# Kernel tuning notes

Hardware: AMD Instinct MI355X
Metric: run time of the kernel (lower is better)

Reference implementation:

```python
import jax, jax.numpy as jnp
import numpy as np

N = 100000
E = 1600000
F_IN = 128
DIM = 32
NUM_CLASSES = 40
BN_EPS = 1e-5


def setup_inputs() -> dict:
    key = jax.random.key(0)
    ks = jax.random.split(key, 16)
    inp = {}
    inp['x'] = jax.random.normal(ks[0], (N, F_IN), dtype=jnp.float32)
    inp['edge_index'] = jax.random.randint(ks[1], (2, E), 0, N, dtype=jnp.int64)
    s = lambda fan_in: 1.0 / np.sqrt(fan_in)
    # GINConv 1 MLP: Linear(F_IN, DIM) -> ReLU -> Linear(DIM, DIM)
    inp['w1a'] = jax.random.uniform(ks[2], (F_IN, DIM), jnp.float32, -s(F_IN), s(F_IN))
    inp['b1a'] = jnp.zeros((DIM,), jnp.float32)
    inp['w1b'] = jax.random.uniform(ks[3], (DIM, DIM), jnp.float32, -s(DIM), s(DIM))
    inp['b1b'] = jnp.zeros((DIM,), jnp.float32)
    # GINConv 2 MLP: Linear(DIM, DIM) -> ReLU -> Linear(DIM, DIM)
    inp['w2a'] = jax.random.uniform(ks[4], (DIM, DIM), jnp.float32, -s(DIM), s(DIM))
    inp['b2a'] = jnp.zeros((DIM,), jnp.float32)
    inp['w2b'] = jax.random.uniform(ks[5], (DIM, DIM), jnp.float32, -s(DIM), s(DIM))
    inp['b2b'] = jnp.zeros((DIM,), jnp.float32)
    # BatchNorm params (eval mode: running stats)
    inp['bn1_g'] = jnp.ones((DIM,), jnp.float32)
    inp['bn1_b'] = jnp.zeros((DIM,), jnp.float32)
    inp['bn1_m'] = jax.random.normal(ks[6], (DIM,), jnp.float32) * 0.1
    inp['bn1_v'] = jax.random.uniform(ks[7], (DIM,), jnp.float32, 0.5, 1.5)
    inp['bn2_g'] = jnp.ones((DIM,), jnp.float32)
    inp['bn2_b'] = jnp.zeros((DIM,), jnp.float32)
    inp['bn2_m'] = jax.random.normal(ks[8], (DIM,), jnp.float32) * 0.1
    inp['bn2_v'] = jax.random.uniform(ks[9], (DIM,), jnp.float32, 0.5, 1.5)
    # FC heads
    inp['fc1_w'] = jax.random.uniform(ks[10], (DIM, DIM), jnp.float32, -s(DIM), s(DIM))
    inp['fc1_b'] = jnp.zeros((DIM,), jnp.float32)
    inp['fc2_w'] = jax.random.uniform(ks[11], (DIM, NUM_CLASSES), jnp.float32, -s(DIM), s(DIM))
    inp['fc2_b'] = jnp.zeros((NUM_CLASSES,), jnp.float32)
    return inp


def _gin_conv(x, src, dst, wa, ba, wb, bb):
    # sum-aggregate neighbor features (messages flow src -> dst), eps = 0
    agg = jax.ops.segment_sum(x[src], dst, num_segments=N)
    h = agg + x  # (1 + eps) * x + sum_j x_j
    h = jax.nn.relu(h @ wa + ba)
    return h @ wb + bb


def _bn(x, g, b, m, v):
    return (x - m) * (g * jax.lax.rsqrt(v + BN_EPS)) + b


def reference(x, edge_index, w1a, b1a, w1b, b1b, w2a, b2a, w2b, b2b,
              bn1_g, bn1_b, bn1_m, bn1_v, bn2_g, bn2_b, bn2_m, bn2_v,
              fc1_w, fc1_b, fc2_w, fc2_b):
    src, dst = edge_index[0], edge_index[1]
    h = jax.nn.relu(_gin_conv(x, src, dst, w1a, b1a, w1b, b1b))
    h = _bn(h, bn1_g, bn1_b, bn1_m, bn1_v)  # dropout is identity in eval
    h = _gin_conv(h, src, dst, w2a, b2a, w2b, b2b)
    h = _bn(h, bn2_g, bn2_b, bn2_m, bn2_v)
    h = jax.nn.relu(h @ fc1_w + fc1_b)
    logits = h @ fc2_w + fc2_b
    return jax.nn.log_softmax(logits, axis=1)
```

## Files before the change

kernel.cpp:

```cpp
#include <hip/hip_runtime.h>
#include <hip/hip_bf16.h>

static constexpr int N_   = 100000;
static constexpr int E_   = 1600000;
static constexpr int FIN_ = 128;
static constexpr int DIM_ = 32;
static constexpr int NC_  = 40;
static constexpr int NB_BKT = (N_ + 127) / 128;
static constexpr int NCHUNK = 256;
static constexpr int EPC    = E_ / NCHUNK;
static constexpr int PROJ_NB = N_ / 32;
static constexpr int CS_NB  = (NB_BKT + 7) / 8;

__device__ __forceinline__ int edge_at(const void* e, int is64, long long i) {
    return is64 ? (int)((const long long*)e)[i] : ((const int*)e)[i];
}

__device__ __forceinline__ float bflo(unsigned u) { return __uint_as_float(u << 16); }
__device__ __forceinline__ float bfhi(unsigned u) { return __uint_as_float(u & 0xffff0000u); }

#define DETECT_FLAG(edge, sflag)                                        \
    if (threadIdx.x < 64) {                                             \
        const long long* p_ = (const long long*)(edge);                 \
        long long v_ = p_[threadIdx.x];                                 \
        bool bad_ = (v_ < 0 || v_ >= (long long)N_);                    \
        unsigned long long m_ = __ballot(bad_);                         \
        if (threadIdx.x == 0) sflag = (m_ == 0ull) ? 1 : 0;             \
    }                                                                   \
    __syncthreads();

__global__ __launch_bounds__(256) void chist_kernel(const void* __restrict__ edge,
                                                    int* __restrict__ ghist) {
    __shared__ int lh[NB_BKT];
    __shared__ int sflag;
    DETECT_FLAG(edge, sflag)
    for (int i = threadIdx.x; i < NB_BKT; i += 256) lh[i] = 0;
    __syncthreads();
    int f = sflag;
    int b = blockIdx.x;
    int end = b * EPC + EPC;
    for (int e = b * EPC + threadIdx.x; e < end; e += 256) {
        int d = edge_at(edge, f, (long long)E_ + e);
        atomicAdd(&lh[d >> 7], 1);
    }
    __syncthreads();
    for (int i = threadIdx.x; i < NB_BKT; i += 256) ghist[b * NB_BKT + i] = lh[i];
}

__global__ __launch_bounds__(256) void colscan_kernel(const int* __restrict__ ghist,
                                                      int* __restrict__ gcur,
                                                      int* __restrict__ bcnt,
                                                      int* __restrict__ bbase,
                                                      int* __restrict__ offs,
                                                      int* __restrict__ done) {
    __shared__ int tile[256 * 9];
    __shared__ int a[256];
    __shared__ int lastFlag;
    int tid = threadIdx.x;
    int k0 = blockIdx.x * 8;

    {
        int kk = tid & 7, r0 = tid >> 3;
        for (int p = 0; p < 8; ++p) {
            int b = r0 + p * 32;
            int k = k0 + kk;
            tile[b * 9 + kk] = (k < NB_BKT) ? ghist[b * NB_BKT + k] : 0;
        }
    }
    __syncthreads();

    int c = tid >> 5, lane = tid & 31;
    int v[8]; int s = 0;
#pragma unroll
    for (int r = 0; r < 8; ++r) { v[r] = tile[(lane * 8 + r) * 9 + c]; s += v[r]; }
    int incl = s;
#pragma unroll
    for (int off = 1; off < 32; off <<= 1) {
        int u = __shfl_up(incl, off, 32);
        if (lane >= off) incl += u;
    }
    int ex = incl - s;
    int k = k0 + c;
    if (k < NB_BKT) {
        int run = ex;
#pragma unroll
        for (int r = 0; r < 8; ++r) {
            int b = lane * 8 + r;
            gcur[b * NB_BKT + k] = run;
            run += v[r];
        }
        if (lane == 31) bcnt[k] = run;
    }
    __syncthreads();
    if (tid == 0) {
        __threadfence();
        int old = atomicAdd(done, 1);
        lastFlag = (old == CS_NB - 1) ? 1 : 0;
    }
    __syncthreads();
    if (lastFlag) {
        __threadfence();
        int b4[4]; int base4 = tid * 4; int t = 0;
#pragma unroll
        for (int j = 0; j < 4; ++j) { int i = base4 + j; b4[j] = (i < NB_BKT) ? bcnt[i] : 0; t += b4[j]; }
        a[tid] = t;
        __syncthreads();
        for (int off = 1; off < 256; off <<= 1) {
            int u = a[tid] + ((tid >= off) ? a[tid - off] : 0);
            __syncthreads(); a[tid] = u; __syncthreads();
        }
        int g = a[tid] - t;
#pragma unroll
        for (int j = 0; j < 4; ++j) { int i = base4 + j; if (i < NB_BKT) bbase[i] = g; g += b4[j]; }
        if (tid == 255) offs[N_] = a[255];
    }
}

__global__ __launch_bounds__(256) void dscatter_kernel(const void* __restrict__ edge,
                                                       const int* __restrict__ bbase,
                                                       const int* __restrict__ gcur,
                                                       int* __restrict__ packed) {
    __shared__ int cur[NB_BKT];
    __shared__ int sflag;
    DETECT_FLAG(edge, sflag)
    int b = blockIdx.x, tid = threadIdx.x;
    for (int k = tid; k < NB_BKT; k += 256) cur[k] = bbase[k] + gcur[b * NB_BKT + k];
    __syncthreads();
    int f = sflag;
    int end = b * EPC + EPC;
    for (int e = b * EPC + tid; e < end; e += 256) {
        int s = edge_at(edge, f, e);
        int d = edge_at(edge, f, (long long)E_ + e);
        int pos = atomicAdd(&cur[d >> 7], 1);
        packed[pos] = s | ((d & 127) << 17);
    }
}

__global__ __launch_bounds__(256) void fat_kernel(const int* __restrict__ bcnt,
                                                  const int* __restrict__ bbase,
                                                  const int* __restrict__ packed,
                                                  int* __restrict__ offs,
                                                  int* __restrict__ csr,
                                                  const float* __restrict__ x,
                                                  const float* __restrict__ w,
                                                  __hip_bfloat16* __restrict__ yh) {
    __shared__ __align__(16) char smem[32768];
    int tid = threadIdx.x;
    if (blockIdx.x < NB_BKT) {
        int* c   = (int*)smem;
        int* cur = (int*)smem + 128;
        int b = blockIdx.x;
        int beg = bbase[b], cnt = bcnt[b];
        if (tid < 128) c[tid] = 0;
        __syncthreads();
        for (int i = tid; i < cnt; i += 256)
            atomicAdd(&c[packed[beg + i] >> 17], 1);
        __syncthreads();
        int myv = (tid < 128) ? c[tid] : 0;
        for (int off = 1; off < 128; off <<= 1) {
            int t = 0;
            if (tid < 128) t = c[tid] + ((tid >= off) ? c[tid - off] : 0);
            __syncthreads();
            if (tid < 128) c[tid] = t;
            __syncthreads();
        }
        if (tid < 128) {
            int ex = c[tid] - myv;
            cur[tid] = ex;
            int node = b * 128 + tid;
            if (node < N_) offs[node] = beg + ex;
        }
        __syncthreads();
        for (int i = tid; i < cnt; i += 256) {
            int v = packed[beg + i];
            int p = atomicAdd(&cur[v >> 17], 1);
            csr[beg + p] = v & 0x1FFFF;
        }
    } else {
        float* wsm = (float*)smem;
        float* xs  = (float*)(smem + 16384);
        const float4* w4 = (const float4*)w;
        float4* ws4 = (float4*)wsm;
        for (int i = tid; i < FIN_ * DIM_ / 4; i += 256) ws4[i] = w4[i];

        int nodeBase = (blockIdx.x - NB_BKT) * 32;
        const float4* x4 = (const float4*)(x + (size_t)nodeBase * FIN_);
        float4* xs4 = (float4*)xs;
        for (int i = tid; i < 32 * FIN_ / 4; i += 256) xs4[i] = x4[i];
        __syncthreads();

        int d = tid & 31, ns = tid >> 5;
        float acc0 = 0.f, acc1 = 0.f, acc2 = 0.f, acc3 = 0.f;
        const float4* r0 = (const float4*)&xs[(ns +  0) * FIN_];
        const float4* r1 = (const float4*)&xs[(ns +  8) * FIN_];
        const float4* r2 = (const float4*)&xs[(ns + 16) * FIN_];
        const float4* r3 = (const float4*)&xs[(ns + 24) * FIN_];
#pragma unroll
        for (int kc = 0; kc < FIN_ / 4; ++kc) {
            float w0 = wsm[(kc * 4 + 0) * DIM_ + d];
            float w1 = wsm[(kc * 4 + 1) * DIM_ + d];
            float w2 = wsm[(kc * 4 + 2) * DIM_ + d];
            float w3 = wsm[(kc * 4 + 3) * DIM_ + d];
            float4 a;
            a = r0[kc]; acc0 += a.x * w0 + a.y * w1 + a.z * w2 + a.w * w3;
            a = r1[kc]; acc1 += a.x * w0 + a.y * w1 + a.z * w2 + a.w * w3;
            a = r2[kc]; acc2 += a.x * w0 + a.y * w1 + a.z * w2 + a.w * w3;
            a = r3[kc]; acc3 += a.x * w0 + a.y * w1 + a.z * w2 + a.w * w3;
        }
        __hip_bfloat16* yo = yh + (size_t)nodeBase * DIM_ + d;
        yo[(ns +  0) * DIM_] = __float2bfloat16(acc0);
        yo[(ns +  8) * DIM_] = __float2bfloat16(acc1);
        yo[(ns + 16) * DIM_] = __float2bfloat16(acc2);
        yo[(ns + 24) * DIM_] = __float2bfloat16(acc3);
    }
}

__device__ __forceinline__ void gather_row(const int* __restrict__ csr,
                                           const char* __restrict__ vb,
                                           int beg, int end, int loff,
                                           float& a0, float& a1, float& a2, float& a3) {
    int i = beg;
    for (; i + 3 < end; i += 4) {
        int s0 = csr[i], s1 = csr[i + 1], s2 = csr[i + 2], s3 = csr[i + 3];
        uint2 u0 = *(const uint2*)(vb + (((size_t)s0) << 6) + loff);
        uint2 u1 = *(const uint2*)(vb + (((size_t)s1) << 6) + loff);
        uint2 u2 = *(const uint2*)(vb + (((size_t)s2) << 6) + loff);
        uint2 u3 = *(const uint2*)(vb + (((size_t)s3) << 6) + loff);
        a0 += (bflo(u0.x) + bflo(u1.x)) + (bflo(u2.x) + bflo(u3.x));
        a1 += (bfhi(u0.x) + bfhi(u1.x)) + (bfhi(u2.x) + bfhi(u3.x));
        a2 += (bflo(u0.y) + bflo(u1.y)) + (bflo(u2.y) + bflo(u3.y));
        a3 += (bfhi(u0.y) + bfhi(u1.y)) + (bfhi(u2.y) + bfhi(u3.y));
    }
    for (; i < end; ++i) {
        int s0 = csr[i];
        uint2 u0 = *(const uint2*)(vb + (((size_t)s0) << 6) + loff);
        a0 += bflo(u0.x); a1 += bfhi(u0.x); a2 += bflo(u0.y); a3 += bfhi(u0.y);
    }
}

__global__ __launch_bounds__(256) void aggmlp1_kernel(const int* __restrict__ offs,
                                                      const int* __restrict__ csr,
                                                      const __hip_bfloat16* __restrict__ yh,
                                                      const float* __restrict__ b1a,
                                                      const float* __restrict__ w1b,
                                                      const float* __restrict__ b1b,
                                                      const float* __restrict__ g1,
                                                      const float* __restrict__ be1,
                                                      const float* __restrict__ m1,
                                                      const float* __restrict__ v1,
                                                      const float* __restrict__ w2a,
                                                      __hip_bfloat16* __restrict__ zh) {
    __shared__ __align__(16) float A[32 * 36];
    __shared__ __align__(16) float B[32 * 36];
    __shared__ float w1s[DIM_ * DIM_];
    __shared__ float w2s[DIM_ * DIM_];
    int tid = threadIdx.x;
    for (int i = tid; i < DIM_ * DIM_; i += 256) { w1s[i] = w1b[i]; w2s[i] = w2a[i]; }

    int nl = tid >> 3, lane = tid & 7;
    int node = blockIdx.x * 32 + nl;
    int beg = offs[node], end = offs[node + 1];
    float a0 = 0.f, a1 = 0.f, a2 = 0.f, a3 = 0.f;
    gather_row(csr, (const char*)yh, beg, end, lane << 3, a0, a1, a2, a3);
    {
        float* p = &A[nl * 36 + lane * 4];
        p[0] = a0; p[1] = a1; p[2] = a2; p[3] = a3;
    }
    __syncthreads();

    int d = tid & 31, ng = tid >> 5;
    size_t gbase = (size_t)blockIdx.x * 32 * DIM_;

    {
        float bv = b1a[d];
#pragma unroll
        for (int r = 0; r < 4; ++r) {
            int n = r * 8 + ng;
            float yv = __bfloat162float(yh[gbase + n * DIM_ + d]);
            A[n * 36 + d] = fmaxf(A[n * 36 + d] + yv + bv, 0.f);
        }
    }
    __syncthreads();

    float sc1 = g1[d] * rsqrtf(v1[d] + 1e-5f);
    float sh1 = be1[d] - m1[d] * sc1;

    {
        float s0 = b1b[d], s1 = s0, s2 = s0, s3 = s0;
        const float4* r0 = (const float4*)&A[(ng +  0) * 36];
        const float4* r1 = (const float4*)&A[(ng +  8) * 36];
        const float4* r2 = (const float4*)&A[(ng + 16) * 36];
        const float4* r3 = (const float4*)&A[(ng + 24) * 36];
#pragma unroll
        for (int kc = 0; kc < 8; ++kc) {
            float w0 = w1s[(kc * 4 + 0) * DIM_ + d];
            float w1 = w1s[(kc * 4 + 1) * DIM_ + d];
            float w2 = w1s[(kc * 4 + 2) * DIM_ + d];
            float w3 = w1s[(kc * 4 + 3) * DIM_ + d];
            float4 a;
            a = r0[kc]; s0 += a.x * w0 + a.y * w1 + a.z * w2 + a.w * w3;
            a = r1[kc]; s1 += a.x * w0 + a.y * w1 + a.z * w2 + a.w * w3;
            a = r2[kc]; s2 += a.x * w0 + a.y * w1 + a.z * w2 + a.w * w3;
            a = r3[kc]; s3 += a.x * w0 + a.y * w1 + a.z * w2 + a.w * w3;
        }
        B[(ng +  0) * 36 + d] = fmaxf(s0, 0.f) * sc1 + sh1;
        B[(ng +  8) * 36 + d] = fmaxf(s1, 0.f) * sc1 + sh1;
        B[(ng + 16) * 36 + d] = fmaxf(s2, 0.f) * sc1 + sh1;
        B[(ng + 24) * 36 + d] = fmaxf(s3, 0.f) * sc1 + sh1;
    }
    __syncthreads();

    {
        float s0 = 0.f, s1 = 0.f, s2 = 0.f, s3 = 0.f;
        const float4* r0 = (const float4*)&B[(ng +  0) * 36];
        const float4* r1 = (const float4*)&B[(ng +  8) * 36];
        const float4* r2 = (const float4*)&B[(ng + 16) * 36];
        const float4* r3 = (const float4*)&B[(ng + 24) * 36];
#pragma unroll
        for (int kc = 0; kc < 8; ++kc) {
            float w0 = w2s[(kc * 4 + 0) * DIM_ + d];
            float w1 = w2s[(kc * 4 + 1) * DIM_ + d];
            float w2 = w2s[(kc * 4 + 2) * DIM_ + d];
            float w3 = w2s[(kc * 4 + 3) * DIM_ + d];
            float4 a;
            a = r0[kc]; s0 += a.x * w0 + a.y * w1 + a.z * w2 + a.w * w3;
            a = r1[kc]; s1 += a.x * w0 + a.y * w1 + a.z * w2 + a.w * w3;
            a = r2[kc]; s2 += a.x * w0 + a.y * w1 + a.z * w2 + a.w * w3;
            a = r3[kc]; s3 += a.x * w0 + a.y * w1 + a.z * w2 + a.w * w3;
        }
        zh[gbase + (ng +  0) * DIM_ + d] = __float2bfloat16(s0);
        zh[gbase + (ng +  8) * DIM_ + d] = __float2bfloat16(s1);
        zh[gbase + (ng + 16) * DIM_ + d] = __float2bfloat16(s2);
        zh[gbase + (ng + 24) * DIM_ + d] = __float2bfloat16(s3);
    }
}

__global__ __launch_bounds__(256) void aggmlp2_kernel(const int* __restrict__ offs,
                                                      const int* __restrict__ csr,
                                                      const __hip_bfloat16* __restrict__ zh,
                                                      const float* __restrict__ b2a,
                                                      const float* __restrict__ w2b,
                                                      const float* __restrict__ b2b,
                                                      const float* __restrict__ g2,
                                                      const float* __restrict__ be2,
                                                      const float* __restrict__ m2,
                                                      const float* __restrict__ v2,
                                                      const float* __restrict__ f1w,
                                                      const float* __restrict__ f1b,
                                                      const float* __restrict__ f2w,
                                                      const float* __restrict__ f2b,
                                                      float* __restrict__ out) {
    __shared__ __align__(16) float A[32 * 36];
    __shared__ __align__(16) float BC[DIM_ * NC_];
    __shared__ float wA[DIM_ * DIM_];
    __shared__ float wB[DIM_ * DIM_];
    int tid = threadIdx.x;
    for (int i = tid; i < DIM_ * DIM_; i += 256) { wA[i] = w2b[i]; wB[i] = f1w[i]; }

    int nl = tid >> 3, lane = tid & 7;
    int node = blockIdx.x * 32 + nl;
    int beg = offs[node], end = offs[node + 1];
    float a0 = 0.f, a1 = 0.f, a2 = 0.f, a3 = 0.f;
    gather_row(csr, (const char*)zh, beg, end, lane << 3, a0, a1, a2, a3);
    {
        float* p = &A[nl * 36 + lane * 4];
        p[0] = a0; p[1] = a1; p[2] = a2; p[3] = a3;
    }
    __syncthreads();

    int d = tid & 31, ng = tid >> 5;
    size_t gbase = (size_t)blockIdx.x * 32 * DIM_;

    {
        float bv = b2a[d];
#pragma unroll
        for (int r = 0; r < 4; ++r) {
            int n = r * 8 + ng;
            float zv = __bfloat162float(zh[gbase + n * DIM_ + d]);
            A[n * 36 + d] = fmaxf(A[n * 36 + d] + zv + bv, 0.f);
        }
    }
    __syncthreads();

    float sc2 = g2[d] * rsqrtf(v2[d] + 1e-5f);
    float sh2 = be2[d] - m2[d] * sc2;

    {
        float s0 = b2b[d], s1 = s0, s2 = s0, s3 = s0;
        const float4* r0 = (const float4*)&A[(ng +  0) * 36];
        const float4* r1 = (const float4*)&A[(ng +  8) * 36];
        const float4* r2 = (const float4*)&A[(ng + 16) * 36];
        const float4* r3 = (const float4*)&A[(ng + 24) * 36];
#pragma unroll
        for (int kc = 0; kc < 8; ++kc) {
            float w0 = wA[(kc * 4 + 0) * DIM_ + d];
            float w1 = wA[(kc * 4 + 1) * DIM_ + d];
            float w2 = wA[(kc * 4 + 2) * DIM_ + d];
            float w3 = wA[(kc * 4 + 3) * DIM_ + d];
            float4 a;
            a = r0[kc]; s0 += a.x * w0 + a.y * w1 + a.z * w2 + a.w * w3;
            a = r1[kc]; s1 += a.x * w0 + a.y * w1 + a.z * w2 + a.w * w3;
            a = r2[kc]; s2 += a.x * w0 + a.y * w1 + a.z * w2 + a.w * w3;
            a = r3[kc]; s3 += a.x * w0 + a.y * w1 + a.z * w2 + a.w * w3;
        }
        BC[(ng +  0) * 36 + d] = s0 * sc2 + sh2;
        BC[(ng +  8) * 36 + d] = s1 * sc2 + sh2;
        BC[(ng + 16) * 36 + d] = s2 * sc2 + sh2;
        BC[(ng + 24) * 36 + d] = s3 * sc2 + sh2;
    }
    __syncthreads();

    {
        float s0 = f1b[d], s1 = s0, s2 = s0, s3 = s0;
        const float4* r0 = (const float4*)&BC[(ng +  0) * 36];
        const float4* r1 = (const float4*)&BC[(ng +  8) * 36];
        const float4* r2 = (const float4*)&BC[(ng + 16) * 36];
        const float4* r3 = (const float4*)&BC[(ng + 24) * 36];
#pragma unroll
        for (int kc = 0; kc < 8; ++kc) {
            float w0 = wB[(kc * 4 + 0) * DIM_ + d];
            float w1 = wB[(kc * 4 + 1) * DIM_ + d];
            float w2 = wB[(kc * 4 + 2) * DIM_ + d];
            float w3 = wB[(kc * 4 + 3) * DIM_ + d];
            float4 a;
            a = r0[kc]; s0 += a.x * w0 + a.y * w1 + a.z * w2 + a.w * w3;
            a = r1[kc]; s1 += a.x * w0 + a.y * w1 + a.z * w2 + a.w * w3;
            a = r2[kc]; s2 += a.x * w0 + a.y * w1 + a.z * w2 + a.w * w3;
            a = r3[kc]; s3 += a.x * w0 + a.y * w1 + a.z * w2 + a.w * w3;
        }
        A[(ng +  0) * 36 + d] = fmaxf(s0, 0.f);
        A[(ng +  8) * 36 + d] = fmaxf(s1, 0.f);
        A[(ng + 16) * 36 + d] = fmaxf(s2, 0.f);
        A[(ng + 24) * 36 + d] = fmaxf(s3, 0.f);
    }
    __syncthreads();
    for (int i = tid; i < DIM_ * NC_; i += 256) BC[i] = f2w[i];
    __syncthreads();

    int c2 = 32 + (d & 7);
    float l00 = f2b[d], l01 = l00, l02 = l00, l03 = l00;
    float cb = f2b[c2];
    float l10 = cb, l11 = cb, l12 = cb, l13 = cb;
    {
        const float4* r0 = (const float4*)&A[(ng +  0) * 36];
        const float4* r1 = (const float4*)&A[(ng +  8) * 36];
        const float4* r2 = (const float4*)&A[(ng + 16) * 36];
        const float4* r3 = (const float4*)&A[(ng + 24) * 36];
#pragma unroll
        for (int kc = 0; kc < 8; ++kc) {
            float wa0 = BC[(kc * 4 + 0) * NC_ + d];
            float wa1 = BC[(kc * 4 + 1) * NC_ + d];
            float wa2 = BC[(kc * 4 + 2) * NC_ + d];
            float wa3 = BC[(kc * 4 + 3) * NC_ + d];
            float wb0 = BC[(kc * 4 + 0) * NC_ + c2];
            float wb1 = BC[(kc * 4 + 1) * NC_ + c2];
            float wb2 = BC[(kc * 4 + 2) * NC_ + c2];
            float wb3 = BC[(kc * 4 + 3) * NC_ + c2];
            float4 a;
            a = r0[kc];
            l00 += a.x * wa0 + a.y * wa1 + a.z * wa2 + a.w * wa3;
            l10 += a.x * wb0 + a.y * wb1 + a.z * wb2 + a.w * wb3;
            a = r1[kc];
            l01 += a.x * wa0 + a.y * wa1 + a.z * wa2 + a.w * wa3;
            l11 += a.x * wb0 + a.y * wb1 + a.z * wb2 + a.w * wb3;
            a = r2[kc];
            l02 += a.x * wa0 + a.y * wa1 + a.z * wa2 + a.w * wa3;
            l12 += a.x * wb0 + a.y * wb1 + a.z * wb2 + a.w * wb3;
            a = r3[kc];
            l03 += a.x * wa0 + a.y * wa1 + a.z * wa2 + a.w * wa3;
            l13 += a.x * wb0 + a.y * wb1 + a.z * wb2 + a.w * wb3;
        }
    }
#pragma unroll
    for (int r = 0; r < 4; ++r) {
        float l0 = (r == 0) ? l00 : (r == 1) ? l01 : (r == 2) ? l02 : l03;
        float l1 = (r == 0) ? l10 : (r == 1) ? l11 : (r == 2) ? l12 : l13;
        int n = r * 8 + ng;
        float mx = fmaxf(l0, l1);
#pragma unroll
        for (int off = 16; off; off >>= 1) mx = fmaxf(mx, __shfl_xor(mx, off));
        float se = __expf(l0 - mx) + ((d < 8) ? __expf(l1 - mx) : 0.f);
#pragma unroll
        for (int off = 16; off; off >>= 1) se += __shfl_xor(se, off);
        float lse = mx + __logf(se);
        size_t ob = (size_t)(blockIdx.x * 32 + n) * NC_;
        out[ob + d] = l0 - lse;
        if (d < 8) out[ob + 32 + d] = l1 - lse;
    }
}

extern "C" void kernel_launch(void* const* d_in, const int* in_sizes, int n_in,
                              void* d_out, int out_size, void* d_ws, size_t ws_size,
                              hipStream_t stream) {
    const float* x   = (const float*)d_in[0];
    const void*  edg = d_in[1];
    const float* w1a = (const float*)d_in[2];
    const float* b1a = (const float*)d_in[3];
    const float* w1b = (const float*)d_in[4];
    const float* b1b = (const float*)d_in[5];
    const float* w2a = (const float*)d_in[6];
    const float* b2a = (const float*)d_in[7];
    const float* w2b = (const float*)d_in[8];
    const float* b2b = (const float*)d_in[9];
    const float* g1  = (const float*)d_in[10];
    const float* be1 = (const float*)d_in[11];
    const float* m1  = (const float*)d_in[12];
    const float* v1  = (const float*)d_in[13];
    const float* g2  = (const float*)d_in[14];
    const float* be2 = (const float*)d_in[15];
    const float* m2  = (const float*)d_in[16];
    const float* v2  = (const float*)d_in[17];
    const float* f1w = (const float*)d_in[18];
    const float* f1b = (const float*)d_in[19];
    const float* f2w = (const float*)d_in[20];
    const float* f2b = (const float*)d_in[21];
    float* out = (float*)d_out;

    char* ws = (char*)d_ws;
    int* done   = (int*)ws;
    int* bcnt   = (int*)(ws + 256);
    int* bbase  = (int*)(ws + 3584);
    int* ghist  = (int*)(ws + 6912);
    int* gcur   = (int*)(ws + 807680);
    int* offs   = (int*)(ws + 1608448);
    int* packed = (int*)(ws + 2008576);
    int* csr    = (int*)(ws + 8408576);
    __hip_bfloat16* yh = (__hip_bfloat16*)(ws + 14808576);
    __hip_bfloat16* zh = (__hip_bfloat16*)(ws + 21208576);

    hipMemsetAsync(done, 0, 4, stream);

    chist_kernel<<<NCHUNK, 256, 0, stream>>>(edg, ghist);
    colscan_kernel<<<CS_NB, 256, 0, stream>>>(ghist, gcur, bcnt, bbase, offs, done);
    dscatter_kernel<<<NCHUNK, 256, 0, stream>>>(edg, bbase, gcur, packed);
    fat_kernel<<<NB_BKT + PROJ_NB, 256, 0, stream>>>(bcnt, bbase, packed, offs, csr,
                                                     x, w1a, yh);

    aggmlp1_kernel<<<N_ / 32, 256, 0, stream>>>(offs, csr, yh, b1a, w1b, b1b,
                                                g1, be1, m1, v1, w2a, zh);

    aggmlp2_kernel<<<N_ / 32, 256, 0, stream>>>(offs, csr, zh, b2a, w2b, b2b,
                                                g2, be2, m2, v2, f1w, f1b,
                                                f2w, f2b, out);
}
```

Before: 312.6 us.

## Split fused gather+MLP kernels into separate gather and MLP kernels

Each fused aggregate+MLP kernel is split in two. A lightweight gather kernel sums neighbour rows, adds the self row and bias, applies ReLU and writes fp32 rows to a workspace buffer. A separate MLP kernel then reads those rows into shared memory. The gather kernel uses no shared memory or weight loads, which may raise occupancy for the latency-bound gather, at the cost of two extra launches and an extra 12.8 MB fp32 write and read per layer.

```diff
diff --git a/kernel.cpp b/kernel.cpp
--- a/kernel.cpp
+++ b/kernel.cpp
@@ -238,49 +238,50 @@
     }
 }
 
-__global__ __launch_bounds__(256) void aggmlp1_kernel(const int* __restrict__ offs,
-                                                      const int* __restrict__ csr,
-                                                      const __hip_bfloat16* __restrict__ yh,
-                                                      const float* __restrict__ b1a,
-                                                      const float* __restrict__ w1b,
-                                                      const float* __restrict__ b1b,
-                                                      const float* __restrict__ g1,
-                                                      const float* __restrict__ be1,
-                                                      const float* __restrict__ m1,
-                                                      const float* __restrict__ v1,
-                                                      const float* __restrict__ w2a,
-                                                      __hip_bfloat16* __restrict__ zh) {
+__global__ __launch_bounds__(256) void gathu_kernel(const int* __restrict__ offs,
+                                                    const int* __restrict__ csr,
+                                                    const __hip_bfloat16* __restrict__ vh,
+                                                    const float* __restrict__ bias,
+                                                    float* __restrict__ u) {
+    int tid = threadIdx.x;
+    int nl = tid >> 3, slot = tid & 7;
+    int node = blockIdx.x * 32 + nl;
+    int beg = offs[node], end = offs[node + 1];
+    float a0 = 0.f, a1 = 0.f, a2 = 0.f, a3 = 0.f;
+    gather_row(csr, (const char*)vh, beg, end, slot << 3, a0, a1, a2, a3);
+    uint2 uy = *(const uint2*)((const char*)vh + (((size_t)node) << 6) + (slot << 3));
+    float4 bv = ((const float4*)bias)[slot];
+    float4 r;
+    r.x = fmaxf(a0 + bflo(uy.x) + bv.x, 0.f);
+    r.y = fmaxf(a1 + bfhi(uy.x) + bv.y, 0.f);
+    r.z = fmaxf(a2 + bflo(uy.y) + bv.z, 0.f);
+    r.w = fmaxf(a3 + bfhi(uy.y) + bv.w, 0.f);
+    ((float4*)u)[(size_t)blockIdx.x * 256 + tid] = r;
+}
+
+__global__ __launch_bounds__(256) void mlp1_kernel(const float* __restrict__ u,
+                                                   const float* __restrict__ w1b,
+                                                   const float* __restrict__ b1b,
+                                                   const float* __restrict__ g1,
+                                                   const float* __restrict__ be1,
+                                                   const float* __restrict__ m1,
+                                                   const float* __restrict__ v1,
+                                                   const float* __restrict__ w2a,
+                                                   __hip_bfloat16* __restrict__ zh) {
     __shared__ __align__(16) float A[32 * 36];
     __shared__ __align__(16) float B[32 * 36];
     __shared__ float w1s[DIM_ * DIM_];
     __shared__ float w2s[DIM_ * DIM_];
     int tid = threadIdx.x;
     for (int i = tid; i < DIM_ * DIM_; i += 256) { w1s[i] = w1b[i]; w2s[i] = w2a[i]; }
-
-    int nl = tid >> 3, lane = tid & 7;
-    int node = blockIdx.x * 32 + nl;
-    int beg = offs[node], end = offs[node + 1];
-    float a0 = 0.f, a1 = 0.f, a2 = 0.f, a3 = 0.f;
-    gather_row(csr, (const char*)yh, beg, end, lane << 3, a0, a1, a2, a3);
-    {
-        float* p = &A[nl * 36 + lane * 4];
-        p[0] = a0; p[1] = a1; p[2] = a2; p[3] = a3;
+    {
+        int n = tid >> 3, sl = tid & 7;
+        *(float4*)&A[n * 36 + sl * 4] = ((const float4*)u)[(size_t)blockIdx.x * 256 + tid];
     }
     __syncthreads();
 
     int d = tid & 31, ng = tid >> 5;
     size_t gbase = (size_t)blockIdx.x * 32 * DIM_;
-
-    {
-        float bv = b1a[d];
-#pragma unroll
-        for (int r = 0; r < 4; ++r) {
-            int n = r * 8 + ng;
-            float yv = __bfloat162float(yh[gbase + n * DIM_ + d]);
-            A[n * 36 + d] = fmaxf(A[n * 36 + d] + yv + bv, 0.f);
-        }
-    }
-    __syncthreads();
 
     float sc1 = g1[d] * rsqrtf(v1[d] + 1e-5f);
     float sh1 = be1[d] - m1[d] * sc1;
@@ -335,52 +336,31 @@
     }
 }
 
-__global__ __launch_bounds__(256) void aggmlp2_kernel(const int* __restrict__ offs,
-                                                      const int* __restrict__ csr,
-                                                      const __hip_bfloat16* __restrict__ zh,
-                                                      const float* __restrict__ b2a,
-                                                      const float* __restrict__ w2b,
-                                                      const float* __restrict__ b2b,
-                                                      const float* __restrict__ g2,
-                                                      const float* __restrict__ be2,
-                                                      const float* __restrict__ m2,
-                                                      const float* __restrict__ v2,
-                                                      const float* __restrict__ f1w,
-                                                      const float* __restrict__ f1b,
-                                                      const float* __restrict__ f2w,
-                                                      const float* __restrict__ f2b,
-                                                      float* __restrict__ out) {
+__global__ __launch_bounds__(256) void mlp2_kernel(const float* __restrict__ u,
+                                                   const float* __restrict__ w2b,
+                                                   const float* __restrict__ b2b,
+                                                   const float* __restrict__ g2,
+                                                   const float* __restrict__ be2,
+                                                   const float* __restrict__ m2,
+                                                   const float* __restrict__ v2,
+                                                   const float* __restrict__ f1w,
+                                                   const float* __restrict__ f1b,
+                                                   const float* __restrict__ f2w,
+                                                   const float* __restrict__ f2b,
+                                                   float* __restrict__ out) {
     __shared__ __align__(16) float A[32 * 36];
     __shared__ __align__(16) float BC[DIM_ * NC_];
     __shared__ float wA[DIM_ * DIM_];
     __shared__ float wB[DIM_ * DIM_];
     int tid = threadIdx.x;
     for (int i = tid; i < DIM_ * DIM_; i += 256) { wA[i] = w2b[i]; wB[i] = f1w[i]; }
-
-    int nl = tid >> 3, lane = tid & 7;
-    int node = blockIdx.x * 32 + nl;
-    int beg = offs[node], end = offs[node + 1];
-    float a0 = 0.f, a1 = 0.f, a2 = 0.f, a3 = 0.f;
-    gather_row(csr, (const char*)zh, beg, end, lane << 3, a0, a1, a2, a3);
-    {
-        float* p = &A[nl * 36 + lane * 4];
-        p[0] = a0; p[1] = a1; p[2] = a2; p[3] = a3;
+    {
+        int n = tid >> 3, sl = tid & 7;
+        *(float4*)&A[n * 36 + sl * 4] = ((const float4*)u)[(size_t)blockIdx.x * 256 + tid];
     }
     __syncthreads();
 
     int d = tid & 31, ng = tid >> 5;
-    size_t gbase = (size_t)blockIdx.x * 32 * DIM_;
-
-    {
-        float bv = b2a[d];
-#pragma unroll
-        for (int r = 0; r < 4; ++r) {
-            int n = r * 8 + ng;
-            float zv = __bfloat162float(zh[gbase + n * DIM_ + d]);
-            A[n * 36 + d] = fmaxf(A[n * 36 + d] + zv + bv, 0.f);
-        }
-    }
-    __syncthreads();
 
     float sc2 = g2[d] * rsqrtf(v2[d] + 1e-5f);
     float sh2 = be2[d] - m2[d] * sc2;
@@ -527,6 +507,7 @@
     int* csr    = (int*)(ws + 8408576);
     __hip_bfloat16* yh = (__hip_bfloat16*)(ws + 14808576);
     __hip_bfloat16* zh = (__hip_bfloat16*)(ws + 21208576);
+    float* u    = (float*)(ws + 27608576);
 
     hipMemsetAsync(done, 0, 4, stream);
 
@@ -536,10 +517,10 @@
     fat_kernel<<<NB_BKT + PROJ_NB, 256, 0, stream>>>(bcnt, bbase, packed, offs, csr,
                                                      x, w1a, yh);
 
-    aggmlp1_kernel<<<N_ / 32, 256, 0, stream>>>(offs, csr, yh, b1a, w1b, b1b,
-                                                g1, be1, m1, v1, w2a, zh);
-
-    aggmlp2_kernel<<<N_ / 32, 256, 0, stream>>>(offs, csr, zh, b2a, w2b, b2b,
-                                                g2, be2, m2, v2, f1w, f1b,
-                                                f2w, f2b, out);
-}
+    gathu_kernel<<<N_ / 32, 256, 0, stream>>>(offs, csr, yh, b1a, u);
+    mlp1_kernel<<<N_ / 32, 256, 0, stream>>>(u, w1b, b1b, g1, be1, m1, v1, w2a, zh);
+
+    gathu_kernel<<<N_ / 32, 256, 0, stream>>>(offs, csr, zh, b2a, u);
+    mlp2_kernel<<<N_ / 32, 256, 0, stream>>>(u, w2b, b2b, g2, be2, m2, v2,
+                                             f1w, f1b, f2w, f2b, out);
+}
```

Result: faster. 303.7 us (-2.8%).
